# Kernel optimization log

Measured on AMD Instinct MI355X. Metric: run time of the kernel, lower is better.

Reference implementation:

```python
import jax, jax.numpy as jnp
import numpy as np

B, L, D_MODEL = 2, 2048, 2048
D_INNER, D_STATE, D_CONV, DT_RANK = 4096, 16, 4, 128


def setup_inputs() -> dict:
    key = jax.random.key(0)
    ks = jax.random.split(key, 8)
    s = 0.02
    return {
        "hidden_states": jax.random.normal(ks[0], (B, L, D_MODEL), jnp.float32),
        "in_proj_weight": jax.random.normal(ks[1], (2 * D_INNER, D_MODEL), jnp.float32) * s,
        "conv1d_weight": jax.random.normal(ks[2], (D_INNER, 1, D_CONV), jnp.float32) * s,
        "conv1d_bias": jnp.zeros((D_INNER,), jnp.float32),
        "x_proj_weight": jax.random.normal(ks[3], (DT_RANK + 2 * D_STATE, D_INNER), jnp.float32) * s,
        "dt_proj_weight": jax.random.normal(ks[4], (D_INNER, DT_RANK), jnp.float32) * s,
        "dt_proj_bias": jax.random.uniform(ks[5], (D_INNER,), jnp.float32, -4.0, -2.0),
        "out_proj_weight": jax.random.normal(ks[6], (D_MODEL, D_INNER), jnp.float32) * s,
        # real Mamba init: A_log = log(1..d_state) broadcast over channels
        "A_log": jnp.log(jnp.broadcast_to(jnp.arange(1, D_STATE + 1, dtype=jnp.float32), (D_INNER, D_STATE))),
        "D": jnp.ones((D_INNER,), jnp.float32),
    }


def reference(hidden_states, in_proj_weight, conv1d_weight, conv1d_bias,
              x_proj_weight, dt_proj_weight, dt_proj_bias, out_proj_weight,
              A_log, D):
    negA = -jnp.exp(A_log)  # [d_inner, d_state]
    # in_proj (no bias) then transpose(1,2): [B, 2*d_inner, L]
    xz = jnp.einsum('bld,ed->bel', hidden_states, in_proj_weight)
    x, z = jnp.split(xz, 2, axis=1)  # each [B, d_inner, L]
    # causal depthwise conv1d + silu
    x = jax.lax.conv_general_dilated(
        x, conv1d_weight, window_strides=(1,), padding=[(D_CONV - 1, 0)],
        dimension_numbers=('NCH', 'OIH', 'NCH'), feature_group_count=D_INNER,
    ) + conv1d_bias[None, :, None]
    x = jax.nn.silu(x)
    xT = x.transpose(0, 2, 1)  # [B, L, d_inner]
    # x_proj -> (dt_rank, d_state, d_state)
    x_dbl = jnp.einsum('bld,ed->ble', xT, x_proj_weight)
    dt_lo = x_dbl[..., :DT_RANK]
    Bm = x_dbl[..., DT_RANK:DT_RANK + D_STATE]   # [B, L, n]
    Cm = x_dbl[..., DT_RANK + D_STATE:]          # [B, L, n]
    # dt_proj + delta_bias, softplus (delta_softplus=True)
    dt = jax.nn.softplus(jnp.einsum('blr,dr->bld', dt_lo, dt_proj_weight) + dt_proj_bias)

    # selective scan: h_t = exp(dt_t*A)*h_{t-1} + dt_t*x_t*B_t ; y_t = C_t . h_t
    def step(h, inp):
        dt_t, B_t, C_t, x_t = inp  # [B,d],[B,n],[B,n],[B,d]
        dA = jnp.exp(dt_t[..., None] * negA)           # [B, d, n]
        h = h * dA + (dt_t * x_t)[..., None] * B_t[:, None, :]
        y = jnp.einsum('bdn,bn->bd', h, C_t)
        return h, y

    h0 = jnp.zeros((B, D_INNER, D_STATE), dt.dtype)
    _, ys = jax.lax.scan(
        step, h0,
        (dt.transpose(1, 0, 2), Bm.transpose(1, 0, 2),
         Cm.transpose(1, 0, 2), xT.transpose(1, 0, 2)),
    )  # ys: [L, B, d_inner]
    y = ys.transpose(1, 0, 2) + xT * D          # skip connection D*x
    y = y * jax.nn.silu(z.transpose(0, 2, 1))   # gate
    # out_proj (no bias): [B, L, d_model]
    return jnp.einsum('bld,ed->ble', y, out_proj_weight)
```

## Files before the change

### kernel.cpp

```cpp
#include <hip/hip_runtime.h>
#include <math.h>

#define B_ 2
#define L_ 2048
#define DMODEL 2048
#define DINNER 4096
#define DSTATE 16
#define DCONV 4
#define DTRANK 128
#define NCHUNK 32
#define CLEN 64
#define MROWS 4096

typedef unsigned short ushort_t;
typedef unsigned int uint_t;
typedef __attribute__((ext_vector_type(8))) short bf16x8;
typedef __attribute__((ext_vector_type(4))) float floatx4;

__device__ __forceinline__ float sigmoidf_(float x){ return 1.f/(1.f+__expf(-x)); }
__device__ __forceinline__ ushort_t f2bf(float f){
    uint_t u = __builtin_bit_cast(uint_t, f);
    return (ushort_t)((u + 0x7FFFu + ((u >> 16) & 1u)) >> 16);
}
__device__ __forceinline__ float bf2f(ushort_t h){
    return __builtin_bit_cast(float, (uint_t)h << 16);
}
__device__ __forceinline__ float fast_exp2(float x){
#if __has_builtin(__builtin_amdgcn_exp2f)
    return __builtin_amdgcn_exp2f(x);
#else
    return exp2f(x);
#endif
}
#define LOG2E 1.44269504088896f

#define GLD_LDS16(g, l) __builtin_amdgcn_global_load_lds( \
    (const __attribute__((address_space(1))) void*)(g),   \
    (__attribute__((address_space(3))) void*)(l), 16, 0, 0)

template<int OUTBF, int EPI, int SPLIT, int KSPLIT>
__global__ __launch_bounds__(256)
void gemm_mfma(const ushort_t* __restrict__ Aptr, int lda,
               const ushort_t* __restrict__ W, int ldw,
               void* __restrict__ Cptr, void* __restrict__ C2,
               int ldc, int Klen,
               const float* __restrict__ bias)
{
    __shared__ ushort_t lsA[128*64];
    __shared__ ushort_t lsW[128*64];
    const int tid  = threadIdx.x;
    const int row0 = blockIdx.x * 128;
    const int col0 = blockIdx.y * 128;
    const int koff = KSPLIT ? blockIdx.z * Klen : 0;
    const int lane = tid & 63;
    const int wv   = tid >> 6;
    const int wm   = (wv >> 1) * 64;
    const int wn   = (wv & 1) * 64;
    const int lr   = lane & 15;
    const int lq   = lane >> 4;

    floatx4 acc[4][4];
    #pragma unroll
    for(int i=0;i<4;i++)
        #pragma unroll
        for(int j=0;j<4;j++)
            #pragma unroll
            for(int r=0;r<4;r++) acc[i][j][r] = 0.f;

    for(int k0 = koff; k0 < koff + Klen; k0 += 64){
        #pragma unroll
        for(int it=0; it<4; it++){
            const int slot = it*256 + tid;
            const int row  = slot >> 3;
            const int p    = slot & 7;
            const int s    = p ^ (row & 7);
            const ushort_t* gw = W    + (size_t)(col0 + row)*ldw + k0 + s*8;
            const ushort_t* ga = Aptr + (size_t)(row0 + row)*lda + k0 + s*8;
            GLD_LDS16(gw, &lsW[slot*8]);
            GLD_LDS16(ga, &lsA[slot*8]);
        }
        __syncthreads();

        #pragma unroll
        for(int kk=0; kk<2; kk++){
            bf16x8 af[4], bw[4];
            #pragma unroll
            for(int i=0;i<4;i++){
                const int ra = wm + i*16 + lr;
                const int rb = wn + i*16 + lr;
                af[i] = *(const bf16x8*)&lsA[ra*64 + (((kk*4+lq) ^ (ra&7))*8)];
                bw[i] = *(const bf16x8*)&lsW[rb*64 + (((kk*4+lq) ^ (rb&7))*8)];
            }
            #pragma unroll
            for(int i=0;i<4;i++)
                #pragma unroll
                for(int j=0;j<4;j++)
                    acc[i][j] = __builtin_amdgcn_mfma_f32_16x16x32_bf16(af[i], bw[j], acc[i][j], 0, 0, 0);
        }
        __syncthreads();
    }

    void* dst = Cptr;
    int cbase = col0;
    if (SPLIT && col0 >= ldc){ dst = C2; cbase = col0 - ldc; }
    const size_t zoff = KSPLIT ? (size_t)blockIdx.z * MROWS * ldc : 0;

    #pragma unroll
    for(int i=0;i<4;i++){
        #pragma unroll
        for(int r=0;r<4;r++){
            const int row = row0 + wm + i*16 + lq*4 + r;
            #pragma unroll
            for(int j=0;j<4;j++){
                const int col = cbase + wn + j*16 + lr;
                float v = acc[i][j][r];
                if (EPI){
                    v += bias[col];
                    v = (v > 20.f) ? v : log1pf(expf(v));
                }
                if (OUTBF) ((ushort_t*)dst)[(size_t)row*ldc + col] = f2bf(v);
                else       ((float*)  dst)[zoff + (size_t)row*ldc + col] = v;
            }
        }
    }
}

template<int OUTBF, int SPLIT, int KSPLIT>
__global__ __launch_bounds__(1024, 4)
void gemm_256w(const ushort_t* __restrict__ Aptr, int lda,
               const ushort_t* __restrict__ W, int ldw,
               void* __restrict__ Cptr, void* __restrict__ C2,
               int ldc, int Klen)
{
    __shared__ ushort_t lds[3][2][8192];
    const int tid  = threadIdx.x;
    const int row0 = blockIdx.x * 256;
    const int col0 = blockIdx.y * 256;
    const int koff = KSPLIT ? blockIdx.z * Klen : 0;
    const int NT   = Klen >> 5;
    const int lane = tid & 63;
    const int wv   = tid >> 6;
    const int wr   = wv >> 2;
    const int wc   = wv & 3;
    const int lr   = lane & 15;
    const int lq   = lane >> 4;

    const int srow = tid >> 2;
    const int sc   = (tid & 3) ^ ((srow >> 1) & 3);
    const ushort_t* aS = Aptr + (size_t)(row0 + srow)*lda + sc*8;
    const ushort_t* wS = W    + (size_t)(col0 + srow)*ldw + sc*8;
    const int sdst = tid*8;

    const int rA = wr*64 + lr;
    const int rB = wc*64 + lr;
    const int aA = rA*32 + ((lq ^ ((rA>>1)&3))*8);
    const int aB = rB*32 + ((lq ^ ((rB>>1)&3))*8);

    floatx4 acc[4][4];
    #pragma unroll
    for(int i=0;i<4;i++)
        #pragma unroll
        for(int j=0;j<4;j++)
            #pragma unroll
            for(int r=0;r<4;r++) acc[i][j][r] = 0.f;

    GLD_LDS16(aS + koff,      &lds[0][0][sdst]);
    GLD_LDS16(wS + koff,      &lds[0][1][sdst]);
    GLD_LDS16(aS + koff + 32, &lds[1][0][sdst]);
    GLD_LDS16(wS + koff + 32, &lds[1][1][sdst]);

    int bs = 0;
    for(int t=0; t<NT; ++t){
        if (t+1 < NT) asm volatile("s_waitcnt vmcnt(2)\ns_barrier" ::: "memory");
        else          asm volatile("s_waitcnt vmcnt(0)\ns_barrier" ::: "memory");
        const ushort_t* pA = lds[bs][0];
        const ushort_t* pB = lds[bs][1];
        bf16x8 af[4], bw[4];
        #pragma unroll
        for(int j=0;j<4;j++) bw[j] = *(const bf16x8*)&pB[aB + j*512];
        #pragma unroll
        for(int i=0;i<4;i++) af[i] = *(const bf16x8*)&pA[aA + i*512];
        if (t+2 < NT){
            int b2 = bs + 2; if (b2 >= 3) b2 -= 3;
            const int kc = koff + (t+2)*32;
            GLD_LDS16(aS + kc, &lds[b2][0][sdst]);
            GLD_LDS16(wS + kc, &lds[b2][1][sdst]);
        }
        __builtin_amdgcn_s_setprio(1);
        #pragma unroll
        for(int i=0;i<4;i++)
            #pragma unroll
            for(int j=0;j<4;j++)
                acc[i][j] = __builtin_amdgcn_mfma_f32_16x16x32_bf16(af[i], bw[j], acc[i][j],0,0,0);
        __builtin_amdgcn_s_setprio(0);
        bs = (bs + 1 == 3) ? 0 : bs + 1;
    }

    void* dst = Cptr;
    int cb = col0;
    if (SPLIT && col0 >= ldc){ dst = C2; cb = col0 - ldc; }
    const size_t zoff = KSPLIT ? (size_t)blockIdx.z * MROWS * ldc : 0;
    const int rbase = row0 + wr*64 + lq*4;
    const int cbase = cb + wc*64 + lr;
    #pragma unroll
    for(int i=0;i<4;i++){
        #pragma unroll
        for(int r=0;r<4;r++){
            const int row = rbase + i*16 + r;
            #pragma unroll
            for(int j=0;j<4;j++){
                const int col = cbase + j*16;
                const float v = acc[i][j][r];
                if (OUTBF) ((ushort_t*)dst)[(size_t)row*ldc + col] = f2bf(v);
                else       ((float*)dst)[zoff + (size_t)row*ldc + col] = v;
            }
        }
    }
}

__global__ __launch_bounds__(256)
void cvt_bf16(const float* __restrict__ in, ushort_t* __restrict__ out, int n4)
{
    const int i = blockIdx.x*256 + threadIdx.x;
    if (i < n4){
        float4 v = *(const float4*)(in + (size_t)i*4);
        union { ushort_t u[4]; uint2 q; } p;
        p.u[0]=f2bf(v.x); p.u[1]=f2bf(v.y); p.u[2]=f2bf(v.z); p.u[3]=f2bf(v.w);
        *(uint2*)(out + (size_t)i*4) = p.q;
    }
}

__global__ __launch_bounds__(256)
void cvt_pad256(const float* __restrict__ in, ushort_t* __restrict__ out)
{
    const int i = blockIdx.x*256 + threadIdx.x;
    const int row = i >> 10;
    const int c4  = i & 1023;
    union { ushort_t u[4]; uint2 q; } p;
    if (row < 160){
        float4 v = *(const float4*)(in + (size_t)row*4096 + c4*4);
        p.u[0]=f2bf(v.x); p.u[1]=f2bf(v.y); p.u[2]=f2bf(v.z); p.u[3]=f2bf(v.w);
    } else { p.u[0]=0; p.u[1]=0; p.u[2]=0; p.u[3]=0; }
    *(uint2*)(out + (size_t)i*4) = p.q;
}

__global__ __launch_bounds__(256)
void reduce_xproj(const float* __restrict__ P, float* __restrict__ xdbl,
                  ushort_t* __restrict__ dtlo)
{
    const int row = blockIdx.x;
    const int col = threadIdx.x;
    float s = 0.f;
    #pragma unroll
    for(int z=0; z<8; z++)
        s += P[(size_t)z*MROWS*256 + (size_t)row*256 + col];
    if (col < 160) xdbl[(size_t)row*160 + col] = s;
    if (col < DTRANK) dtlo[(size_t)row*DTRANK + col] = f2bf(s);
}

__global__ __launch_bounds__(256)
void conv_silu_bf(const ushort_t* __restrict__ xb, const float* __restrict__ w,
                  const float* __restrict__ bias, ushort_t* __restrict__ xc)
{
    const int gid = blockIdx.x*256 + threadIdx.x;
    const int d = gid & (DINNER-1);
    const int t = gid >> 12;
    const int l = t & (L_-1);
    float s = bias[d];
    #pragma unroll
    for(int j=0;j<DCONV;j++){
        const int ll = l - (DCONV-1) + j;
        if (ll >= 0)
            s = fmaf(bf2f(xb[(size_t)(t-(DCONV-1)+j)*DINNER + d]), w[d*DCONV+j], s);
    }
    xc[(size_t)t*DINNER + d] = f2bf(s * sigmoidf_(s));
}

__global__ __launch_bounds__(256)
void scan_phase1(const ushort_t* __restrict__ dt_bf,
                 const ushort_t* __restrict__ xconv,
                 const float* __restrict__ xdbl,
                 const float* __restrict__ A_log,
                 float* __restrict__ sc_h, float* __restrict__ sc_S)
{
    const int tid = threadIdx.x;
    const int d = blockIdx.x*256 + tid;
    const int chunk = blockIdx.y;
    const int b = blockIdx.z;
    const int l0 = chunk*CLEN;

    __shared__ float Bs[CLEN][DSTATE];
    for(int i=tid; i<CLEN*DSTATE; i+=256){
        const int row = i >> 4, n = i & 15;
        Bs[row][n] = xdbl[(size_t)(b*L_ + l0 + row)*160 + DTRANK + n];
    }
    float negA[DSTATE];
    #pragma unroll
    for(int n=0;n<DSTATE;n++) negA[n] = -expf(A_log[d*DSTATE + n]) * LOG2E;
    __syncthreads();

    float h[DSTATE], S[DSTATE];
    #pragma unroll
    for(int n=0;n<DSTATE;n++){ h[n]=0.f; S[n]=0.f; }

    size_t idx = (size_t)(b*L_ + l0)*DINNER + d;
    float dt_c = bf2f(dt_bf[idx]);
    float xv_c = bf2f(xconv[idx]);
    for(int l=0;l<CLEN;l++){
        float dt_n = 0.f, xv_n = 0.f;
        if (l+1 < CLEN){
            dt_n = bf2f(dt_bf[idx + DINNER]);
            xv_n = bf2f(xconv[idx + DINNER]);
        }
        const float dx = dt_c * xv_c;
        #pragma unroll
        for(int n=0;n<DSTATE;n++){
            const float t = dt_c * negA[n];
            S[n] += t;
            h[n] = fmaf(h[n], fast_exp2(t), dx*Bs[l][n]);
        }
        dt_c = dt_n; xv_c = xv_n;
        idx += DINNER;
    }
    const size_t o = (size_t)(b*NCHUNK + chunk)*DSTATE*DINNER + d;
    #pragma unroll
    for(int n=0;n<DSTATE;n++){
        sc_h[o + (size_t)n*DINNER] = h[n];
        sc_S[o + (size_t)n*DINNER] = S[n];
    }
}

__global__ __launch_bounds__(256)
void scan_phase2(float* __restrict__ sc_h, const float* __restrict__ sc_S)
{
    const int gid = blockIdx.x*256 + threadIdx.x;
    const int b = gid / (DSTATE*DINNER);
    const int rem = gid - b*DSTATE*DINNER;
    const size_t base = (size_t)b*NCHUNK*DSTATE*DINNER + rem;
    float H = 0.f;
    #pragma unroll
    for(int c=0;c<NCHUNK;c++){
        const size_t idx = base + (size_t)c*DSTATE*DINNER;
        const float he = sc_h[idx];
        const float S  = sc_S[idx];
        sc_h[idx] = H;
        H = fmaf(fast_exp2(S), H, he);
    }
}

__global__ __launch_bounds__(256)
void scan_phase3(const ushort_t* __restrict__ dt_bf,
                 const ushort_t* __restrict__ xconv,
                 const float* __restrict__ xdbl,
                 const ushort_t* __restrict__ z_bf,
                 const float* __restrict__ A_log,
                 const float* __restrict__ Dvec,
                 const float* __restrict__ sc_h,
                 ushort_t* __restrict__ y_bf)
{
    const int tid = threadIdx.x;
    const int d = blockIdx.x*256 + tid;
    const int chunk = blockIdx.y;
    const int b = blockIdx.z;
    const int l0 = chunk*CLEN;

    __shared__ float BCs[CLEN][2*DSTATE];
    for(int i=tid; i<CLEN*2*DSTATE; i+=256){
        const int row = i >> 5, c = i & 31;
        BCs[row][c] = xdbl[(size_t)(b*L_ + l0 + row)*160 + DTRANK + c];
    }
    float negA[DSTATE];
    #pragma unroll
    for(int n=0;n<DSTATE;n++) negA[n] = -expf(A_log[d*DSTATE + n]) * LOG2E;
    const float Dv = Dvec[d];
    float h[DSTATE];
    const size_t o = (size_t)(b*NCHUNK + chunk)*DSTATE*DINNER + d;
    #pragma unroll
    for(int n=0;n<DSTATE;n++) h[n] = sc_h[o + (size_t)n*DINNER];
    __syncthreads();

    size_t idx = (size_t)(b*L_ + l0)*DINNER + d;
    float dt_c = bf2f(dt_bf[idx]);
    float xv_c = bf2f(xconv[idx]);
    float zv_c = bf2f(z_bf[idx]);
    for(int l=0;l<CLEN;l++){
        float dt_n = 0.f, xv_n = 0.f, zv_n = 0.f;
        if (l+1 < CLEN){
            dt_n = bf2f(dt_bf[idx + DINNER]);
            xv_n = bf2f(xconv[idx + DINNER]);
            zv_n = bf2f(z_bf[idx + DINNER]);
        }
        const float dx = dt_c * xv_c;
        float y = 0.f;
        #pragma unroll
        for(int n=0;n<DSTATE;n++){
            const float t = dt_c * negA[n];
            h[n] = fmaf(h[n], fast_exp2(t), dx*BCs[l][n]);
            y = fmaf(h[n], BCs[l][DSTATE+n], y);
        }
        const float g = zv_c * sigmoidf_(zv_c);
        y_bf[idx] = f2bf(fmaf(xv_c, Dv, y) * g);
        dt_c = dt_n; xv_c = xv_n; zv_c = zv_n;
        idx += DINNER;
    }
}

extern "C" void kernel_launch(void* const* d_in, const int* in_sizes, int n_in,
                              void* d_out, int out_size, void* d_ws, size_t ws_size,
                              hipStream_t stream) {
    const float* hs      = (const float*)d_in[0];
    const float* w_in    = (const float*)d_in[1];
    const float* w_conv  = (const float*)d_in[2];
    const float* b_conv  = (const float*)d_in[3];
    const float* w_xproj = (const float*)d_in[4];
    const float* w_dt    = (const float*)d_in[5];
    const float* b_dt    = (const float*)d_in[6];
    const float* w_out   = (const float*)d_in[7];
    const float* A_log   = (const float*)d_in[8];
    const float* Dvec    = (const float*)d_in[9];
    float* out = (float*)d_out;

    char* base = (char*)d_ws;
    ushort_t* x_bf   = (ushort_t*)(base);
    float*    xdbl   = (float*)   (base);
    ushort_t* wx_bf  = (ushort_t*)(base + (4u<<20));
    ushort_t* dtlo_bf= (ushort_t*)(base + (6u<<20));
    ushort_t* wdt_bf = (ushort_t*)(base + (7u<<20));
    float*    sc_h   = (float*)   (base + (8u<<20));
    ushort_t* z_bf   = (ushort_t*)(base + (32u<<20));
    ushort_t* xconv  = (ushort_t*)(base + (64u<<20));
    ushort_t* wi_bf  = (ushort_t*)(base + (96u<<20));
    ushort_t* dt_bf  = (ushort_t*)(base + (96u<<20));
    ushort_t* hs_bf  = (ushort_t*)(base + (128u<<20));
    float*    sc_S   = (float*)   (base + (128u<<20));
    ushort_t* wo_bf  = (ushort_t*)(base + (128u<<20));
    float*    xp_par = (float*)   (base + (144u<<20));
    ushort_t* y_bf   = (ushort_t*)(base + (144u<<20));

    dim3 blk(256);
    dim3 blkW(1024);

    cvt_bf16<<<dim3(MROWS*DMODEL/4/256), blk, 0, stream>>>(hs, hs_bf, MROWS*DMODEL/4);
    cvt_bf16<<<dim3(2*DINNER*DMODEL/4/256), blk, 0, stream>>>(w_in, wi_bf, 2*DINNER*DMODEL/4);

    gemm_256w<1,1,0><<<dim3(MROWS/256, 2*DINNER/256), blkW, 0, stream>>>(
        hs_bf, DMODEL, wi_bf, DMODEL, x_bf, z_bf, DINNER, DMODEL);

    conv_silu_bf<<<dim3((size_t)MROWS*DINNER/256), blk, 0, stream>>>(x_bf, w_conv, b_conv, xconv);

    cvt_pad256<<<dim3(256*4096/4/256), blk, 0, stream>>>(w_xproj, wx_bf);
    gemm_mfma<0,0,0,1><<<dim3(MROWS/128, 2, 8), blk, 0, stream>>>(
        xconv, DINNER, wx_bf, DINNER, xp_par, nullptr, 256, DINNER/8, nullptr);
    reduce_xproj<<<dim3(MROWS), blk, 0, stream>>>(xp_par, xdbl, dtlo_bf);

    cvt_bf16<<<dim3(DINNER*DTRANK/4/256), blk, 0, stream>>>(w_dt, wdt_bf, DINNER*DTRANK/4);
    gemm_mfma<1,1,0,0><<<dim3(MROWS/128, DINNER/128), blk, 0, stream>>>(
        dtlo_bf, DTRANK, wdt_bf, DTRANK, dt_bf, nullptr, DINNER, DTRANK, b_dt);

    dim3 sgrid(DINNER/256, NCHUNK, B_);
    scan_phase1<<<sgrid, blk, 0, stream>>>(dt_bf, xconv, xdbl, A_log, sc_h, sc_S);
    scan_phase2<<<dim3(B_*DSTATE*DINNER/256), blk, 0, stream>>>(sc_h, sc_S);

    cvt_bf16<<<dim3(DMODEL*DINNER/4/256), blk, 0, stream>>>(w_out, wo_bf, DMODEL*DINNER/4);

    scan_phase3<<<sgrid, blk, 0, stream>>>(dt_bf, xconv, xdbl, z_bf, A_log, Dvec, sc_h, y_bf);

    gemm_mfma<0,0,0,0><<<dim3(MROWS/128, DMODEL/128), blk, 0, stream>>>(
        y_bf, DINNER, wo_bf, DINNER, out, nullptr, DMODEL, DINNER, nullptr);
}
```

Before: 689.0 us.

## Deepen GEMM LDS pipeline with register double-buffering and merge conversion launches

The big in_proj GEMM moves from a 3-stage to a 4-stage LDS ring. Fragments are double-buffered in registers so the next tile's LDS reads are issued before the current tile's MFMAs, with a sched_barrier to keep the order. Several small fp32-to-bf16 conversion kernels are merged into combined launches, and the w_out conversion is folded into scan_phase2. This cuts launch overhead and hides LDS latency, at the cost of more LDS and register pressure. y_bf now aliases dt_bf, which drops __restrict__ from scan_phase3 and risks a read/write hazard if dt for a position is read after its y is written.

```diff
diff --git a/kernel.cpp b/kernel.cpp
--- a/kernel.cpp
+++ b/kernel.cpp
@@ -125,18 +125,18 @@
     }
 }
 
-template<int OUTBF, int SPLIT, int KSPLIT>
+template<int OUTBF, int SPLIT>
 __global__ __launch_bounds__(1024, 4)
 void gemm_256w(const ushort_t* __restrict__ Aptr, int lda,
                const ushort_t* __restrict__ W, int ldw,
                void* __restrict__ Cptr, void* __restrict__ C2,
                int ldc, int Klen)
 {
-    __shared__ ushort_t lds[3][2][8192];
+    __shared__ ushort_t lds[4][2][8192];
     const int tid  = threadIdx.x;
     const int row0 = blockIdx.x * 256;
     const int col0 = blockIdx.y * 256;
-    const int koff = KSPLIT ? blockIdx.z * Klen : 0;
+    const int koff = 0;
     const int NT   = Klen >> 5;
     const int lane = tid & 63;
     const int wv   = tid >> 6;
@@ -164,42 +164,57 @@
             #pragma unroll
             for(int r=0;r<4;r++) acc[i][j][r] = 0.f;
 
+    bf16x8 fa0[4], fb0[4], fa1[4], fb1[4];
+
     GLD_LDS16(aS + koff,      &lds[0][0][sdst]);
     GLD_LDS16(wS + koff,      &lds[0][1][sdst]);
     GLD_LDS16(aS + koff + 32, &lds[1][0][sdst]);
     GLD_LDS16(wS + koff + 32, &lds[1][1][sdst]);
-
-    int bs = 0;
-    for(int t=0; t<NT; ++t){
-        if (t+1 < NT) asm volatile("s_waitcnt vmcnt(2)\ns_barrier" ::: "memory");
-        else          asm volatile("s_waitcnt vmcnt(0)\ns_barrier" ::: "memory");
-        const ushort_t* pA = lds[bs][0];
-        const ushort_t* pB = lds[bs][1];
-        bf16x8 af[4], bw[4];
-        #pragma unroll
-        for(int j=0;j<4;j++) bw[j] = *(const bf16x8*)&pB[aB + j*512];
-        #pragma unroll
-        for(int i=0;i<4;i++) af[i] = *(const bf16x8*)&pA[aA + i*512];
-        if (t+2 < NT){
-            int b2 = bs + 2; if (b2 >= 3) b2 -= 3;
-            const int kc = koff + (t+2)*32;
-            GLD_LDS16(aS + kc, &lds[b2][0][sdst]);
-            GLD_LDS16(wS + kc, &lds[b2][1][sdst]);
-        }
-        __builtin_amdgcn_s_setprio(1);
-        #pragma unroll
-        for(int i=0;i<4;i++)
-            #pragma unroll
-            for(int j=0;j<4;j++)
-                acc[i][j] = __builtin_amdgcn_mfma_f32_16x16x32_bf16(af[i], bw[j], acc[i][j],0,0,0);
-        __builtin_amdgcn_s_setprio(0);
-        bs = (bs + 1 == 3) ? 0 : bs + 1;
-    }
+    GLD_LDS16(aS + koff + 64, &lds[2][0][sdst]);
+    GLD_LDS16(wS + koff + 64, &lds[2][1][sdst]);
+    asm volatile("s_waitcnt vmcnt(4)\ns_barrier" ::: "memory");
+    #pragma unroll
+    for(int j=0;j<4;j++) fb0[j] = *(const bf16x8*)&lds[0][1][aB + j*512];
+    #pragma unroll
+    for(int i=0;i<4;i++) fa0[i] = *(const bf16x8*)&lds[0][0][aA + i*512];
+
+    #define BODY(T, FA_C, FB_C, FA_N, FB_N) { \
+        const int t_ = (T); \
+        if (t_+2 < NT)      asm volatile("s_waitcnt vmcnt(2)\ns_barrier" ::: "memory"); \
+        else if (t_+1 < NT) asm volatile("s_waitcnt vmcnt(0)\ns_barrier" ::: "memory"); \
+        if (t_+1 < NT){ \
+            const ushort_t* pA = lds[(t_+1)&3][0]; \
+            const ushort_t* pB = lds[(t_+1)&3][1]; \
+            _Pragma("unroll") \
+            for(int j=0;j<4;j++) FB_N[j] = *(const bf16x8*)&pB[aB + j*512]; \
+            _Pragma("unroll") \
+            for(int i=0;i<4;i++) FA_N[i] = *(const bf16x8*)&pA[aA + i*512]; \
+        } \
+        if (t_+3 < NT){ \
+            const int kc = koff + (t_+3)*32; \
+            GLD_LDS16(aS + kc, &lds[(t_+3)&3][0][sdst]); \
+            GLD_LDS16(wS + kc, &lds[(t_+3)&3][1][sdst]); \
+        } \
+        __builtin_amdgcn_sched_barrier(0); \
+        __builtin_amdgcn_s_setprio(1); \
+        _Pragma("unroll") \
+        for(int i=0;i<4;i++){ \
+            _Pragma("unroll") \
+            for(int j=0;j<4;j++) \
+                acc[i][j] = __builtin_amdgcn_mfma_f32_16x16x32_bf16(FA_C[i], FB_C[j], acc[i][j],0,0,0); \
+        } \
+        __builtin_amdgcn_s_setprio(0); \
+    }
+
+    for(int t=0; t<NT; t+=2){
+        BODY(t,   fa0, fb0, fa1, fb1);
+        BODY(t+1, fa1, fb1, fa0, fb0);
+    }
+    #undef BODY
 
     void* dst = Cptr;
     int cb = col0;
     if (SPLIT && col0 >= ldc){ dst = C2; cb = col0 - ldc; }
-    const size_t zoff = KSPLIT ? (size_t)blockIdx.z * MROWS * ldc : 0;
     const int rbase = row0 + wr*64 + lq*4;
     const int cbase = cb + wc*64 + lr;
     #pragma unroll
@@ -212,36 +227,47 @@
                 const int col = cbase + j*16;
                 const float v = acc[i][j][r];
                 if (OUTBF) ((ushort_t*)dst)[(size_t)row*ldc + col] = f2bf(v);
-                else       ((float*)dst)[zoff + (size_t)row*ldc + col] = v;
+                else       ((float*)dst)[(size_t)row*ldc + col] = v;
             }
         }
     }
 }
 
 __global__ __launch_bounds__(256)
-void cvt_bf16(const float* __restrict__ in, ushort_t* __restrict__ out, int n4)
+void cvt2_bf16(const float* __restrict__ in1, ushort_t* __restrict__ out1, int n1_4,
+               const float* __restrict__ in2, ushort_t* __restrict__ out2, int n2_4)
 {
     const int i = blockIdx.x*256 + threadIdx.x;
-    if (i < n4){
-        float4 v = *(const float4*)(in + (size_t)i*4);
-        union { ushort_t u[4]; uint2 q; } p;
+    const float* in; ushort_t* out; int j;
+    if (i < n1_4){ in = in1; out = out1; j = i; }
+    else if (i < n1_4 + n2_4){ in = in2; out = out2; j = i - n1_4; }
+    else return;
+    float4 v = *(const float4*)(in + (size_t)j*4);
+    union { ushort_t u[4]; uint2 q; } p;
+    p.u[0]=f2bf(v.x); p.u[1]=f2bf(v.y); p.u[2]=f2bf(v.z); p.u[3]=f2bf(v.w);
+    *(uint2*)(out + (size_t)j*4) = p.q;
+}
+
+__global__ __launch_bounds__(256)
+void cvt_xw(const float* __restrict__ wx, ushort_t* __restrict__ wx_bf,
+            const float* __restrict__ wdt, ushort_t* __restrict__ wdt_bf)
+{
+    const int i = blockIdx.x*256 + threadIdx.x;
+    union { ushort_t u[4]; uint2 q; } p;
+    if (i < 262144){
+        const int row = i >> 10;
+        const int c4  = i & 1023;
+        if (row < 160){
+            float4 v = *(const float4*)(wx + (size_t)row*4096 + c4*4);
+            p.u[0]=f2bf(v.x); p.u[1]=f2bf(v.y); p.u[2]=f2bf(v.z); p.u[3]=f2bf(v.w);
+        } else { p.u[0]=0; p.u[1]=0; p.u[2]=0; p.u[3]=0; }
+        *(uint2*)(wx_bf + (size_t)i*4) = p.q;
+    } else {
+        const int j = i - 262144;
+        float4 v = *(const float4*)(wdt + (size_t)j*4);
         p.u[0]=f2bf(v.x); p.u[1]=f2bf(v.y); p.u[2]=f2bf(v.z); p.u[3]=f2bf(v.w);
-        *(uint2*)(out + (size_t)i*4) = p.q;
-    }
-}
-
-__global__ __launch_bounds__(256)
-void cvt_pad256(const float* __restrict__ in, ushort_t* __restrict__ out)
-{
-    const int i = blockIdx.x*256 + threadIdx.x;
-    const int row = i >> 10;
-    const int c4  = i & 1023;
-    union { ushort_t u[4]; uint2 q; } p;
-    if (row < 160){
-        float4 v = *(const float4*)(in + (size_t)row*4096 + c4*4);
-        p.u[0]=f2bf(v.x); p.u[1]=f2bf(v.y); p.u[2]=f2bf(v.z); p.u[3]=f2bf(v.w);
-    } else { p.u[0]=0; p.u[1]=0; p.u[2]=0; p.u[3]=0; }
-    *(uint2*)(out + (size_t)i*4) = p.q;
+        *(uint2*)(wdt_bf + (size_t)j*4) = p.q;
+    }
 }
 
 __global__ __launch_bounds__(256)
@@ -330,10 +356,20 @@
     }
 }
 
-__global__ __launch_bounds__(256)
-void scan_phase2(float* __restrict__ sc_h, const float* __restrict__ sc_S)
-{
-    const int gid = blockIdx.x*256 + threadIdx.x;
+#define CVW 8192
+__global__ __launch_bounds__(256)
+void scan_phase2_cvt(float* __restrict__ sc_h, const float* __restrict__ sc_S,
+                     const float* __restrict__ w_out, ushort_t* __restrict__ wo_bf)
+{
+    if (blockIdx.x < CVW){
+        const int i = blockIdx.x*256 + threadIdx.x;
+        float4 v = *(const float4*)(w_out + (size_t)i*4);
+        union { ushort_t u[4]; uint2 q; } p;
+        p.u[0]=f2bf(v.x); p.u[1]=f2bf(v.y); p.u[2]=f2bf(v.z); p.u[3]=f2bf(v.w);
+        *(uint2*)(wo_bf + (size_t)i*4) = p.q;
+        return;
+    }
+    const int gid = (blockIdx.x - CVW)*256 + threadIdx.x;
     const int b = gid / (DSTATE*DINNER);
     const int rem = gid - b*DSTATE*DINNER;
     const size_t base = (size_t)b*NCHUNK*DSTATE*DINNER + rem;
@@ -349,14 +385,14 @@
 }
 
 __global__ __launch_bounds__(256)
-void scan_phase3(const ushort_t* __restrict__ dt_bf,
+void scan_phase3(const ushort_t* dt_bf,
                  const ushort_t* __restrict__ xconv,
                  const float* __restrict__ xdbl,
                  const ushort_t* __restrict__ z_bf,
                  const float* __restrict__ A_log,
                  const float* __restrict__ Dvec,
                  const float* __restrict__ sc_h,
-                 ushort_t* __restrict__ y_bf)
+                 ushort_t* y_bf)
 {
     const int tid = threadIdx.x;
     const int d = blockIdx.x*256 + tid;
@@ -431,37 +467,37 @@
     ushort_t* xconv  = (ushort_t*)(base + (64u<<20));
     ushort_t* wi_bf  = (ushort_t*)(base + (96u<<20));
     ushort_t* dt_bf  = (ushort_t*)(base + (96u<<20));
+    ushort_t* y_bf   = (ushort_t*)(base + (96u<<20));
     ushort_t* hs_bf  = (ushort_t*)(base + (128u<<20));
     float*    sc_S   = (float*)   (base + (128u<<20));
-    ushort_t* wo_bf  = (ushort_t*)(base + (128u<<20));
     float*    xp_par = (float*)   (base + (144u<<20));
-    ushort_t* y_bf   = (ushort_t*)(base + (144u<<20));
+    ushort_t* wo_bf  = (ushort_t*)(base + (144u<<20));
 
     dim3 blk(256);
     dim3 blkW(1024);
 
-    cvt_bf16<<<dim3(MROWS*DMODEL/4/256), blk, 0, stream>>>(hs, hs_bf, MROWS*DMODEL/4);
-    cvt_bf16<<<dim3(2*DINNER*DMODEL/4/256), blk, 0, stream>>>(w_in, wi_bf, 2*DINNER*DMODEL/4);
-
-    gemm_256w<1,1,0><<<dim3(MROWS/256, 2*DINNER/256), blkW, 0, stream>>>(
+    cvt2_bf16<<<dim3((MROWS*DMODEL/4 + 2*DINNER*DMODEL/4)/256), blk, 0, stream>>>(
+        hs, hs_bf, MROWS*DMODEL/4, w_in, wi_bf, 2*DINNER*DMODEL/4);
+
+    gemm_256w<1,1><<<dim3(MROWS/256, 2*DINNER/256), blkW, 0, stream>>>(
         hs_bf, DMODEL, wi_bf, DMODEL, x_bf, z_bf, DINNER, DMODEL);
 
     conv_silu_bf<<<dim3((size_t)MROWS*DINNER/256), blk, 0, stream>>>(x_bf, w_conv, b_conv, xconv);
 
-    cvt_pad256<<<dim3(256*4096/4/256), blk, 0, stream>>>(w_xproj, wx_bf);
+    cvt_xw<<<dim3((262144 + 131072)/256), blk, 0, stream>>>(w_xproj, wx_bf, w_dt, wdt_bf);
+
     gemm_mfma<0,0,0,1><<<dim3(MROWS/128, 2, 8), blk, 0, stream>>>(
         xconv, DINNER, wx_bf, DINNER, xp_par, nullptr, 256, DINNER/8, nullptr);
     reduce_xproj<<<dim3(MROWS), blk, 0, stream>>>(xp_par, xdbl, dtlo_bf);
 
-    cvt_bf16<<<dim3(DINNER*DTRANK/4/256), blk, 0, stream>>>(w_dt, wdt_bf, DINNER*DTRANK/4);
     gemm_mfma<1,1,0,0><<<dim3(MROWS/128, DINNER/128), blk, 0, stream>>>(
         dtlo_bf, DTRANK, wdt_bf, DTRANK, dt_bf, nullptr, DINNER, DTRANK, b_dt);
 
     dim3 sgrid(DINNER/256, NCHUNK, B_);
     scan_phase1<<<sgrid, blk, 0, stream>>>(dt_bf, xconv, xdbl, A_log, sc_h, sc_S);
-    scan_phase2<<<dim3(B_*DSTATE*DINNER/256), blk, 0, stream>>>(sc_h, sc_S);
-
-    cvt_bf16<<<dim3(DMODEL*DINNER/4/256), blk, 0, stream>>>(w_out, wo_bf, DMODEL*DINNER/4);
+
+    scan_phase2_cvt<<<dim3(CVW + B_*DSTATE*DINNER/256), blk, 0, stream>>>(
+        sc_h, sc_S, w_out, wo_bf);
 
     scan_phase3<<<sgrid, blk, 0, stream>>>(dt_bf, xconv, xdbl, z_bf, A_log, Dvec, sc_h, y_bf);
 
```

Measured after the change: 845.4 us. 1.23x slower.
